# Optimization experiments

Measured on AMD Instinct MI355X. Metric: run time of the kernel, lower is better.

Reference implementation:

```python
import jax, jax.numpy as jnp
import numpy as np

N_HEAD = 12

def setup_inputs() -> dict:
    key = jax.random.key(0)
    ks = jax.random.split(key, 5)
    B, T, C = 2, 2048, 768
    s = 1.0 / np.sqrt(C)
    return {
        "x": jax.random.normal(ks[0], (B, T, C), dtype=jnp.float32),
        "W_qkv": jax.random.normal(ks[1], (C, 3 * C), dtype=jnp.float32) * s,
        "b_qkv": jnp.zeros((3 * C,), dtype=jnp.float32),
        "W_proj": jax.random.normal(ks[2], (C, C), dtype=jnp.float32) * s,
        "b_proj": jnp.zeros((C,), dtype=jnp.float32),
    }

def reference(x, W_qkv, b_qkv, W_proj, b_proj):
    B, T, C = x.shape
    H = N_HEAD
    D = C // H
    qkv = x @ W_qkv + b_qkv                      # [B,T,3C]
    qkv = qkv.reshape(B, T, 3, H, D)
    q = jnp.transpose(qkv[:, :, 0], (0, 2, 1, 3))  # [B,H,T,D]
    k = jnp.transpose(qkv[:, :, 1], (0, 2, 1, 3))
    v = jnp.transpose(qkv[:, :, 2], (0, 2, 1, 3))
    scale = 1.0 / np.sqrt(D).astype(np.float32)
    att = jnp.einsum('bhqd,bhkd->bhqk', q, k) * scale  # [B,H,T,T]
    causal = jnp.tril(jnp.ones((T, T), dtype=bool))
    att = jnp.where(causal, att, -jnp.inf)
    att = jax.nn.softmax(att, axis=-1)
    out = jnp.einsum('bhqk,bhkd->bhqd', att, v)   # [B,H,T,D]
    out = jnp.transpose(out, (0, 2, 1, 3)).reshape(B, T, C)
    return out @ W_proj + b_proj
```

## Files before the change

### kernel.cpp

```cpp
#include <hip/hip_runtime.h>
#include <stdint.h>

typedef short short8 __attribute__((ext_vector_type(8)));
typedef short short4v __attribute__((ext_vector_type(4)));
typedef float f32x4 __attribute__((ext_vector_type(4)));
typedef unsigned int u32x2 __attribute__((ext_vector_type(2)));
typedef unsigned int u32x4 __attribute__((ext_vector_type(4)));
typedef unsigned short u16;
typedef unsigned int u32;

#define T_ 2048
#define QK_SCALE 0.180336878f

__device__ inline u16 f2bf(float f) {
  unsigned u = __builtin_bit_cast(unsigned, f);
  u += 0x7fffu + ((u >> 16) & 1u);
  return (u16)(u >> 16);
}

__device__ inline u32 cvt_pk_bf16(float lo, float hi) {
  u32 r;
  asm("v_cvt_pk_bf16_f32 %0, %1, %2" : "=v"(r) : "v"(lo), "v"(hi));
  return r;
}

__device__ inline f32x4 mfma_bf16(short8 a, short8 b, f32x4 c) {
  return __builtin_amdgcn_mfma_f32_16x16x32_bf16(a, b, c, 0, 0, 0);
}

__device__ inline void gload16(const u16* g, u16* l) {
  __builtin_amdgcn_global_load_lds(
      (const __attribute__((address_space(1))) void*)g,
      (__attribute__((address_space(3))) void*)l, 16, 0, 0);
}


__device__ inline void tile_transpose(const float* __restrict__ W, u16* __restrict__ Wt,
                                      int R, int Ccols, int c0, int r0, int t,
                                      float (*tile)[33]) {
  int tr = t >> 3, tc = (t & 7) * 4;
  float4 v = *(const float4*)&W[(size_t)(r0 + tr) * Ccols + c0 + tc];
  tile[tr][tc + 0] = v.x; tile[tr][tc + 1] = v.y;
  tile[tr][tc + 2] = v.z; tile[tr][tc + 3] = v.w;
  __syncthreads();
  short4v o;
#pragma unroll
  for (int i = 0; i < 4; ++i) o[i] = (short)f2bf(tile[tc + i][tr]);
  *(short4v*)&Wt[(size_t)(c0 + tr) * R + r0 + tc] = o;
}

__global__ __launch_bounds__(256) void prep_kernel(const float* __restrict__ x,
                                                   const float* __restrict__ Wqkv,
                                                   const float* __restrict__ Wproj,
                                                   u16* __restrict__ xb,
                                                   u16* __restrict__ wqkvT,
                                                   u16* __restrict__ wprojT) {
  __shared__ float tile[32][33];
  int bid = blockIdx.x, t = threadIdx.x;
  if (bid < 3072) {
    int i = (bid * 256 + t) * 4;
    float4 v = *(const float4*)&x[i];
    short4v o;
    o[0] = (short)f2bf(v.x); o[1] = (short)f2bf(v.y);
    o[2] = (short)f2bf(v.z); o[3] = (short)f2bf(v.w);
    *(short4v*)&xb[i] = o;
  } else if (bid < 3072 + 1728) {
    int t2 = bid - 3072;
    tile_transpose(Wqkv, wqkvT, 768, 2304, (t2 % 72) * 32, (t2 / 72) * 32, t, tile);
  } else {
    int t3 = bid - 4800;
    tile_transpose(Wproj, wprojT, 768, 768, (t3 % 24) * 32, (t3 / 24) * 32, t, tile);
  }
}


template <int MODE, int MTILE>
__global__ __launch_bounds__(256) void gemm_kernel(const u16* __restrict__ A,
                                                   const u16* __restrict__ Bt,
                                                   const float* __restrict__ bias,
                                                   u16* __restrict__ qb,
                                                   u16* __restrict__ kb,
                                                   u16* __restrict__ vpb,
                                                   float* __restrict__ out) {
  constexpr int MF = MTILE / 32;
  __shared__ u16 S[MTILE * 64 + 8192];
  u16* As = S;
  u16* Bs = S + MTILE * 64;
  int tid = threadIdx.x, w = tid >> 6, l = tid & 63, lg = l >> 4, lr = l & 15;
  int nwg = gridDim.x * gridDim.y;
  int hw = blockIdx.y * gridDim.x + blockIdx.x;
  int logical = (hw & 7) * (nwg >> 3) + (hw >> 3);
  int n0 = (logical % gridDim.x) * 128, m0 = (logical / gridDim.x) * MTILE;
  int wm = (w >> 1) * (MTILE / 2), wn = (w & 1) * 64;
  f32x4 acc[MF][4] = {};
  int rsub = l >> 3;
  int sc = ((l & 7) ^ rsub) * 8;
  for (int kt = 0; kt < 12; ++kt) {
    int k0 = kt * 64;
    __syncthreads();
#pragma unroll
    for (int j = 0; j < MF; ++j) {
      int row = w * (MTILE / 4) + j * 8 + rsub;
      gload16(&A[(size_t)(m0 + row) * 768 + k0 + sc], &As[(w * MF + j) * 512]);
    }
#pragma unroll
    for (int j = 0; j < 4; ++j) {
      int row = w * 32 + j * 8 + rsub;
      gload16(&Bt[(size_t)(n0 + row) * 768 + k0 + sc], &Bs[(w * 4 + j) * 512]);
    }
    __syncthreads();
    short8 a[MF][2], b[4][2];
#pragma unroll
    for (int h = 0; h < 2; ++h) {
#pragma unroll
      for (int mf = 0; mf < MF; ++mf) {
        int cw = ((h * 4 + lg) ^ (lr & 7)) * 8;
        a[mf][h] = *(const short8*)&As[(wm + mf * 16 + lr) * 64 + cw];
      }
#pragma unroll
      for (int nf = 0; nf < 4; ++nf) {
        int cw = ((h * 4 + lg) ^ (lr & 7)) * 8;
        b[nf][h] = *(const short8*)&Bs[(wn + nf * 16 + lr) * 64 + cw];
      }
    }
#pragma unroll
    for (int h = 0; h < 2; ++h)
#pragma unroll
      for (int mf = 0; mf < MF; ++mf)
#pragma unroll
        for (int nf = 0; nf < 4; ++nf)
          acc[mf][nf] = mfma_bf16(a[mf][h], b[nf][h], acc[mf][nf]);
  }

  if constexpr (MODE == 0) {
    int sec = (n0 >= 1536) ? 2 : (n0 >= 768 ? 1 : 0);
    int ncol0 = n0 - sec * 768;
    if (sec < 2) {
#pragma unroll
      for (int nf = 0; nf < 4; ++nf) {
        int nn = wn + nf * 16 + lr;
        float bv = bias[n0 + nn];
        int c = ncol0 + nn;
        int hh = c >> 6, d = c & 63;
#pragma unroll
        for (int mf = 0; mf < MF; ++mf)
#pragma unroll
          for (int rr = 0; rr < 4; ++rr) {
            int m = m0 + wm + mf * 16 + 4 * lg + rr;
            int bb = m >> 11, tt = m & 2047;
            int bh = bb * 12 + hh;
            float v = acc[mf][nf][rr] + bv;
            if (sec == 0) qb[((size_t)bh * T_ + tt) * 64 + d] = f2bf(v * QK_SCALE);
            else          kb[((size_t)bh * T_ + tt) * 64 + d] = f2bf(v);
          }
      }
    } else {
      __syncthreads();
#pragma unroll
      for (int nf = 0; nf < 4; ++nf) {
        int row = wn + nf * 16 + lr;
        float bv = bias[n0 + row];
        int swz = (row & 7) << 3;
#pragma unroll
        for (int mf = 0; mf < MF; ++mf) {
          int pcol0 = wm + (mf >> 1) * 32 + 8 * lg + 4 * (mf & 1);
          u32x2 pk;
          pk[0] = cvt_pk_bf16(acc[mf][nf][0] + bv, acc[mf][nf][1] + bv);
          pk[1] = cvt_pk_bf16(acc[mf][nf][2] + bv, acc[mf][nf][3] + bv);
          *(u32x2*)&S[row * MTILE + (pcol0 ^ swz)] = pk;
        }
      }
      __syncthreads();
      constexpr int CPT = MTILE / 2;
      int rowo = tid >> 1, half = tid & 1;
      int c = ncol0 + rowo;
      int d = c & 63, hh = c >> 6;
      int bh = (m0 >> 11) * 12 + hh;
      u16* dst = vpb + ((size_t)bh * 64 + d) * T_ + (m0 & 2047) + half * CPT;
      int swzo = (rowo & 7) << 3;
#pragma unroll
      for (int i = 0; i < CPT / 8; ++i) {
        int col = half * CPT + i * 8;
        uint4 v = *(const uint4*)&S[rowo * MTILE + (col ^ swzo)];
        *(uint4*)&dst[i * 8] = v;
      }
    }
  } else {
#pragma unroll
    for (int nf = 0; nf < 4; ++nf) {
      int n = n0 + wn + nf * 16 + lr;
      float bv = bias[n];
#pragma unroll
      for (int mf = 0; mf < MF; ++mf)
#pragma unroll
        for (int rr = 0; rr < 4; ++rr) {
          int m = m0 + wm + mf * 16 + 4 * lg + rr;
          out[(size_t)m * 768 + n] = acc[mf][nf][rr] + bv;
        }
    }
  }
}


__global__ __launch_bounds__(512) void attn_kernel(const u16* __restrict__ Q,
                                                   const u16* __restrict__ K,
                                                   const u16* __restrict__ Vp,
                                                   u16* __restrict__ O) {
  __shared__ u16 sh[16384];
  int tid = threadIdx.x;
  int w = tid >> 6, l = tid & 63, lg = l >> 4, lr = l & 15;
  int i = w >> 1, j = w & 1;
  int idx = blockIdx.x;
  int head = idx % 24;
  int qblk = 31 - idx / 24;
  int b = head / 12, h = head % 12;
  int q0 = qblk * 64;
  int q0w = q0 + i * 16;
  const u16* Qb = Q + (size_t)head * T_ * 64;
  const u16* Kb = K + (size_t)head * T_ * 64;
  const u16* Vb = Vp + (size_t)head * 64 * T_;

  short8 qf0 = *(const short8*)&Qb[(size_t)(q0w + lr) * 64 + 8 * lg];
  short8 qf1 = *(const short8*)&Qb[(size_t)(q0w + lr) * 64 + 32 + 8 * lg];

  f32x4 ao[4] = {};
  float lrow = 0.f;
  int rsub = l >> 3;
  int scs = ((l & 7) ^ rsub) * 8;
  const int nt = qblk + 1;

  {
    int row = w * 8 + rsub;
    gload16(&Kb[(size_t)row * 64 + scs], &sh[w * 512]);
    gload16(&Vb[(size_t)row * T_ + scs], &sh[8192 + w * 512]);
  }
  __syncthreads();

  for (int t = 0; t < nt; ++t) {
    int cur = t & 1;
    int k0 = t * 64;
    if (t + 1 < nt) {
      int k1 = k0 + 64;
      int row = w * 8 + rsub;
      gload16(&Kb[(size_t)(k1 + row) * 64 + scs], &sh[(cur ^ 1) * 4096 + w * 512]);
      gload16(&Vb[(size_t)row * T_ + k1 + scs], &sh[8192 + (cur ^ 1) * 4096 + w * 512]);
    }
    if (k0 + 32 * j <= q0w + 15) {
      const u16* ks = sh + cur * 4096;
      const u16* vs = sh + 8192 + cur * 4096;
      short8 ka0[2], ka1[2], va[4];
#pragma unroll
      for (int g = 0; g < 2; ++g) {
        int kg = 2 * j + g;
        ka0[g] = *(const short8*)&ks[(kg * 16 + lr) * 64 + ((lg ^ (lr & 7)) * 8)];
        ka1[g] = *(const short8*)&ks[(kg * 16 + lr) * 64 + (((4 + lg) ^ (lr & 7)) * 8)];
      }
#pragma unroll
      for (int dt = 0; dt < 4; ++dt)
        va[dt] = *(const short8*)&vs[(dt * 16 + lr) * 64 + (((4 * j + lg) ^ (lr & 7)) * 8)];
      f32x4 sm[2];
      __builtin_amdgcn_s_setprio(1);
#pragma unroll
      for (int g = 0; g < 2; ++g) {
        f32x4 z = {};
        z = mfma_bf16(ka0[g], qf0, z);
        z = mfma_bf16(ka1[g], qf1, z);
        sm[g] = z;
      }
      __builtin_amdgcn_s_setprio(0);
      float sv[8];
      float ps = 0.f;
      bool needmask = (t == nt - 1) && (32 * j + 31 > 16 * i);
      if (needmask) {
        int qa = q0w + lr;
#pragma unroll
        for (int g = 0; g < 2; ++g)
#pragma unroll
          for (int rr = 0; rr < 4; ++rr) {
            int key = k0 + (2 * j + g) * 16 + 4 * lg + rr;
            float x = (key <= qa) ? sm[g][rr] : -1e30f;
            float p = __builtin_amdgcn_exp2f(x);
            sv[g * 4 + rr] = p;
            ps += p;
          }
      } else {
#pragma unroll
        for (int g = 0; g < 2; ++g)
#pragma unroll
          for (int rr = 0; rr < 4; ++rr) {
            float p = __builtin_amdgcn_exp2f(sm[g][rr]);
            sv[g * 4 + rr] = p;
            ps += p;
          }
      }
      lrow += ps;
      u32x4 uu;
      uu[0] = cvt_pk_bf16(sv[0], sv[1]);
      uu[1] = cvt_pk_bf16(sv[2], sv[3]);
      uu[2] = cvt_pk_bf16(sv[4], sv[5]);
      uu[3] = cvt_pk_bf16(sv[6], sv[7]);
      short8 pb = __builtin_bit_cast(short8, uu);
      __builtin_amdgcn_s_setprio(1);
#pragma unroll
      for (int dt = 0; dt < 4; ++dt)
        ao[dt] = mfma_bf16(va[dt], pb, ao[dt]);
      __builtin_amdgcn_s_setprio(0);
    }
    __syncthreads();
  }

  lrow += __shfl_xor(lrow, 16);
  lrow += __shfl_xor(lrow, 32);

  float* aoL = (float*)sh;
  float* lrL = (float*)(sh + 8192);
  if (j == 1) {
#pragma unroll
    for (int dt = 0; dt < 4; ++dt)
      *(f32x4*)&aoL[(i * 64 + l) * 16 + dt * 4] = ao[dt];
    lrL[i * 64 + l] = lrow;
  }
  __syncthreads();
  if (j == 0) {
#pragma unroll
    for (int dt = 0; dt < 4; ++dt)
      ao[dt] += *(const f32x4*)&aoL[(i * 64 + l) * 16 + dt * 4];
    lrow += lrL[i * 64 + l];
    u16* ow = sh + 9216 + i * 1152;
    float inv = 1.0f / lrow;
#pragma unroll
    for (int dt = 0; dt < 4; ++dt) {
      u32x2 pk;
      pk[0] = cvt_pk_bf16(ao[dt][0] * inv, ao[dt][1] * inv);
      pk[1] = cvt_pk_bf16(ao[dt][2] * inv, ao[dt][3] * inv);
      *(u32x2*)&ow[lr * 72 + dt * 16 + 4 * lg] = pk;
    }
    asm volatile("s_waitcnt lgkmcnt(0)" ::: "memory");
    int r = l >> 2, hc = l & 3;
    const u16* srow = sh + 9216 + i * 1152 + r * 72 + hc * 16;
    u16* dst = O + ((size_t)(b * T_ + q0w + r)) * 768 + h * 64 + hc * 16;
    *(uint4*)&dst[0] = *(const uint4*)&srow[0];
    *(uint4*)&dst[8] = *(const uint4*)&srow[8];
  }
}


extern "C" void kernel_launch(void* const* d_in, const int* in_sizes, int n_in,
                              void* d_out, int out_size, void* d_ws, size_t ws_size,
                              hipStream_t stream) {
  const float* x     = (const float*)d_in[0];
  const float* Wqkv  = (const float*)d_in[1];
  const float* bqkv  = (const float*)d_in[2];
  const float* Wproj = (const float*)d_in[3];
  const float* bproj = (const float*)d_in[4];
  float* out = (float*)d_out;
  char* ws = (char*)d_ws;
  u16* xb     = (u16*)(ws);
  u16* wqkvT  = (u16*)(ws + 6291456);
  u16* wprojT = (u16*)(ws + 9830400);
  u16* qb     = (u16*)(ws + 11010048);
  u16* kb     = (u16*)(ws + 17301504);
  u16* vpb    = (u16*)(ws + 23592960);
  u16* ob     = (u16*)(ws + 29884416);

  prep_kernel<<<5376, 256, 0, stream>>>(x, Wqkv, Wproj, xb, wqkvT, wprojT);
  gemm_kernel<0, 64><<<dim3(18, 64), 256, 0, stream>>>(xb, wqkvT, bqkv, qb, kb, vpb, nullptr);
  attn_kernel<<<768, 512, 0, stream>>>(qb, kb, vpb, ob);
  gemm_kernel<1, 32><<<dim3(6, 128), 256, 0, stream>>>(ob, wprojT, bproj, nullptr, nullptr, nullptr, out);
}
```

Baseline: 76.75 us.

## Process two KV tiles per barrier with double-buffered pairs in attention

```diff
diff --git a/kernel.cpp b/kernel.cpp
--- a/kernel.cpp
+++ b/kernel.cpp
@@ -206,7 +206,7 @@
                                                    const u16* __restrict__ K,
                                                    const u16* __restrict__ Vp,
                                                    u16* __restrict__ O) {
-  __shared__ u16 sh[16384];
+  __shared__ u16 sh[32768];
   int tid = threadIdx.x;
   int w = tid >> 6, l = tid & 63, lg = l >> 4, lr = l & 15;
   int i = w >> 1, j = w & 1;
@@ -227,84 +227,96 @@
   float lrow = 0.f;
   int rsub = l >> 3;
   int scs = ((l & 7) ^ rsub) * 8;
+  int row = w * 8 + rsub;
   const int nt = qblk + 1;
 
-  {
-    int row = w * 8 + rsub;
-    gload16(&Kb[(size_t)row * 64 + scs], &sh[w * 512]);
-    gload16(&Vb[(size_t)row * T_ + scs], &sh[8192 + w * 512]);
+  gload16(&Kb[(size_t)row * 64 + scs], &sh[w * 512]);
+  gload16(&Vb[(size_t)row * T_ + scs], &sh[16384 + w * 512]);
+  if (nt > 1) {
+    gload16(&Kb[(size_t)(64 + row) * 64 + scs], &sh[4096 + w * 512]);
+    gload16(&Vb[(size_t)row * T_ + 64 + scs], &sh[16384 + 4096 + w * 512]);
   }
   __syncthreads();
 
-  for (int t = 0; t < nt; ++t) {
-    int cur = t & 1;
-    int k0 = t * 64;
-    if (t + 1 < nt) {
-      int k1 = k0 + 64;
-      int row = w * 8 + rsub;
-      gload16(&Kb[(size_t)(k1 + row) * 64 + scs], &sh[(cur ^ 1) * 4096 + w * 512]);
-      gload16(&Vb[(size_t)row * T_ + k1 + scs], &sh[8192 + (cur ^ 1) * 4096 + w * 512]);
-    }
-    if (k0 + 32 * j <= q0w + 15) {
-      const u16* ks = sh + cur * 4096;
-      const u16* vs = sh + 8192 + cur * 4096;
-      short8 ka0[2], ka1[2], va[4];
-#pragma unroll
-      for (int g = 0; g < 2; ++g) {
-        int kg = 2 * j + g;
-        ka0[g] = *(const short8*)&ks[(kg * 16 + lr) * 64 + ((lg ^ (lr & 7)) * 8)];
-        ka1[g] = *(const short8*)&ks[(kg * 16 + lr) * 64 + (((4 + lg) ^ (lr & 7)) * 8)];
-      }
-#pragma unroll
-      for (int dt = 0; dt < 4; ++dt)
-        va[dt] = *(const short8*)&vs[(dt * 16 + lr) * 64 + (((4 * j + lg) ^ (lr & 7)) * 8)];
-      f32x4 sm[2];
-      __builtin_amdgcn_s_setprio(1);
-#pragma unroll
-      for (int g = 0; g < 2; ++g) {
-        f32x4 z = {};
-        z = mfma_bf16(ka0[g], qf0, z);
-        z = mfma_bf16(ka1[g], qf1, z);
-        sm[g] = z;
-      }
-      __builtin_amdgcn_s_setprio(0);
-      float sv[8];
-      float ps = 0.f;
-      bool needmask = (t == nt - 1) && (32 * j + 31 > 16 * i);
-      if (needmask) {
-        int qa = q0w + lr;
-#pragma unroll
-        for (int g = 0; g < 2; ++g)
-#pragma unroll
-          for (int rr = 0; rr < 4; ++rr) {
-            int key = k0 + (2 * j + g) * 16 + 4 * lg + rr;
-            float x = (key <= qa) ? sm[g][rr] : -1e30f;
-            float p = __builtin_amdgcn_exp2f(x);
-            sv[g * 4 + rr] = p;
-            ps += p;
+  for (int tp = 0; tp < nt; tp += 2) {
+    int p = (tp >> 1) & 1;
+    if (tp + 2 < nt) {
+      int base = ((p ^ 1) * 2) * 4096;
+      gload16(&Kb[(size_t)((tp + 2) * 64 + row) * 64 + scs], &sh[base + w * 512]);
+      gload16(&Vb[(size_t)row * T_ + (tp + 2) * 64 + scs], &sh[16384 + base + w * 512]);
+    }
+    if (tp + 3 < nt) {
+      int base = ((p ^ 1) * 2 + 1) * 4096;
+      gload16(&Kb[(size_t)((tp + 3) * 64 + row) * 64 + scs], &sh[base + w * 512]);
+      gload16(&Vb[(size_t)row * T_ + (tp + 3) * 64 + scs], &sh[16384 + base + w * 512]);
+    }
+#pragma unroll
+    for (int sub = 0; sub < 2; ++sub) {
+      int t = tp + sub;
+      if (t < nt) {
+        int k0 = t * 64;
+        if (k0 + 32 * j <= q0w + 15) {
+          const u16* ks = sh + (p * 2 + sub) * 4096;
+          const u16* vs = sh + 16384 + (p * 2 + sub) * 4096;
+          short8 ka0[2], ka1[2], va[4];
+#pragma unroll
+          for (int g = 0; g < 2; ++g) {
+            int kg = 2 * j + g;
+            ka0[g] = *(const short8*)&ks[(kg * 16 + lr) * 64 + ((lg ^ (lr & 7)) * 8)];
+            ka1[g] = *(const short8*)&ks[(kg * 16 + lr) * 64 + (((4 + lg) ^ (lr & 7)) * 8)];
           }
-      } else {
-#pragma unroll
-        for (int g = 0; g < 2; ++g)
-#pragma unroll
-          for (int rr = 0; rr < 4; ++rr) {
-            float p = __builtin_amdgcn_exp2f(sm[g][rr]);
-            sv[g * 4 + rr] = p;
-            ps += p;
+#pragma unroll
+          for (int dt = 0; dt < 4; ++dt)
+            va[dt] = *(const short8*)&vs[(dt * 16 + lr) * 64 + (((4 * j + lg) ^ (lr & 7)) * 8)];
+          f32x4 sm[2];
+          __builtin_amdgcn_s_setprio(1);
+#pragma unroll
+          for (int g = 0; g < 2; ++g) {
+            f32x4 z = {};
+            z = mfma_bf16(ka0[g], qf0, z);
+            z = mfma_bf16(ka1[g], qf1, z);
+            sm[g] = z;
           }
-      }
-      lrow += ps;
-      u32x4 uu;
-      uu[0] = cvt_pk_bf16(sv[0], sv[1]);
-      uu[1] = cvt_pk_bf16(sv[2], sv[3]);
-      uu[2] = cvt_pk_bf16(sv[4], sv[5]);
-      uu[3] = cvt_pk_bf16(sv[6], sv[7]);
-      short8 pb = __builtin_bit_cast(short8, uu);
-      __builtin_amdgcn_s_setprio(1);
-#pragma unroll
-      for (int dt = 0; dt < 4; ++dt)
-        ao[dt] = mfma_bf16(va[dt], pb, ao[dt]);
-      __builtin_amdgcn_s_setprio(0);
+          __builtin_amdgcn_s_setprio(0);
+          float sv[8];
+          float ps = 0.f;
+          bool needmask = (t == nt - 1) && (32 * j + 31 > 16 * i);
+          if (needmask) {
+            int qa = q0w + lr;
+#pragma unroll
+            for (int g = 0; g < 2; ++g)
+#pragma unroll
+              for (int rr = 0; rr < 4; ++rr) {
+                int key = k0 + (2 * j + g) * 16 + 4 * lg + rr;
+                float x = (key <= qa) ? sm[g][rr] : -1e30f;
+                float pv = __builtin_amdgcn_exp2f(x);
+                sv[g * 4 + rr] = pv;
+                ps += pv;
+              }
+          } else {
+#pragma unroll
+            for (int g = 0; g < 2; ++g)
+#pragma unroll
+              for (int rr = 0; rr < 4; ++rr) {
+                float pv = __builtin_amdgcn_exp2f(sm[g][rr]);
+                sv[g * 4 + rr] = pv;
+                ps += pv;
+              }
+          }
+          lrow += ps;
+          u32x4 uu;
+          uu[0] = cvt_pk_bf16(sv[0], sv[1]);
+          uu[1] = cvt_pk_bf16(sv[2], sv[3]);
+          uu[2] = cvt_pk_bf16(sv[4], sv[5]);
+          uu[3] = cvt_pk_bf16(sv[6], sv[7]);
+          short8 pb = __builtin_bit_cast(short8, uu);
+          __builtin_amdgcn_s_setprio(1);
+#pragma unroll
+          for (int dt = 0; dt < 4; ++dt)
+            ao[dt] = mfma_bf16(va[dt], pb, ao[dt]);
+          __builtin_amdgcn_s_setprio(0);
+        }
+      }
     }
     __syncthreads();
   }
```

After: 73.96 us. 1.04x faster.
